# Optimization experiments

Measured on AMD Instinct MI355X. Metric: run time of the kernel, lower is better.

Reference implementation:

```python
import jax, jax.numpy as jnp
import numpy as np

N_NODES = 100000
N_EDGES = 3200000
NFEAT, NHID, NCLASS = 512, 256, 40


def spmm(edge_src, edge_dst, edge_w, h):
    # sparse adjacency @ h via gather + weighted segment-sum over destination nodes
    msgs = h[edge_src] * edge_w[:, None]          # [E, d]
    return jax.ops.segment_sum(msgs, edge_dst, num_segments=N_NODES)


def gcn_layer(h, W, b, edge_src, edge_dst, edge_w):
    support = h @ W                                # [N, d_out]
    return spmm(edge_src, edge_dst, edge_w, support) + b


def setup_inputs() -> dict:
    key = jax.random.key(0)
    ks = jax.random.split(key, 16)
    def w(k, shape, fan_in):
        return jax.random.normal(k, shape, dtype=jnp.float32) / np.sqrt(fan_in)
    inp = {
        'x': jax.random.normal(ks[0], (N_NODES, NFEAT), dtype=jnp.float32),
        'W1': w(ks[1], (NFEAT, NHID), NFEAT), 'b1': jnp.zeros((NHID,), jnp.float32),
        'W2': w(ks[2], (NHID, NHID), NHID),  'b2': jnp.zeros((NHID,), jnp.float32),
        'W3': w(ks[3], (NHID, NHID), NHID),  'b3': jnp.zeros((NHID,), jnp.float32),
        'W4': w(ks[4], (NHID, NHID), NHID),  'b4': jnp.zeros((NHID,), jnp.float32),
        'W5': w(ks[5], (NHID, NHID), NHID),  'b5': jnp.zeros((NHID,), jnp.float32),
        'W6': w(ks[6], (NHID, NCLASS), NHID),'b6': jnp.zeros((NCLASS,), jnp.float32),
        'edge_w': jax.random.uniform(ks[7], (N_EDGES,), dtype=jnp.float32),
        'edge_src': jax.random.randint(ks[8], (N_EDGES,), 0, N_NODES, dtype=jnp.int32),
        'edge_dst': jax.random.randint(ks[9], (N_EDGES,), 0, N_NODES, dtype=jnp.int32),
    }
    return inp


def reference(x, W1, b1, W2, b2, W3, b3, W4, b4, W5, b5, W6, b6,
              edge_w, edge_src, edge_dst):
    # eval mode: dropout is identity
    h = jax.nn.relu(gcn_layer(x, W1, b1, edge_src, edge_dst, edge_w))
    h = jax.nn.relu(gcn_layer(h, W2, b2, edge_src, edge_dst, edge_w))
    h = jax.nn.relu(gcn_layer(h, W3, b3, edge_src, edge_dst, edge_w))
    h = jax.nn.relu(gcn_layer(h, W4, b4, edge_src, edge_dst, edge_w))
    h = jax.nn.relu(gcn_layer(h, W5, b5, edge_src, edge_dst, edge_w))
    h = gcn_layer(h, W6, b6, edge_src, edge_dst, edge_w)
    return jax.nn.log_softmax(h, axis=1)
```

## Files before the change

### kernel.cpp

```cpp
#include <hip/hip_runtime.h>
#include <hip/hip_bf16.h>

static const int NN = 100000;
static const int NE = 3200000;
static const int F0 = 512;
static const int FH = 256;
static const int NC = 40;

#define CHUNK_SHIFT 13
static const int NCH  = (NN + (1 << CHUNK_SHIFT) - 1) >> CHUNK_SHIFT;
static const int KEYS = NN * NCH;

#define NPB_SHIFT 8
static const int NPB = 1 << NPB_SHIFT;
static const int NB  = (NN + NPB - 1) >> NPB_SHIFT;
static const int KPB = NPB * NCH;
#define EPB_A 8192

typedef __attribute__((ext_vector_type(8))) short bf16x8;
typedef __attribute__((ext_vector_type(16))) float f32x16;

__device__ __forceinline__ float bf2f(unsigned short u) {
    union { unsigned int i; float f; } c; c.i = ((unsigned int)u) << 16; return c.f;
}
__device__ __forceinline__ unsigned short f2bf(float f) {
    __hip_bfloat16 h = __float2bfloat16(f);
    return *reinterpret_cast<unsigned short*>(&h);
}

__global__ __launch_bounds__(256) void hist_bucket(const int* __restrict__ dst,
                                                   int* __restrict__ bcount, int E) {
    __shared__ int h[NB];
    for (int i = threadIdx.x; i < NB; i += 256) h[i] = 0;
    __syncthreads();
    for (int e = blockIdx.x * 256 + threadIdx.x; e < E; e += gridDim.x * 256)
        atomicAdd(&h[dst[e] >> NPB_SHIFT], 1);
    __syncthreads();
    for (int i = threadIdx.x; i < NB; i += 256)
        if (h[i]) atomicAdd(&bcount[i], h[i]);
}

__global__ __launch_bounds__(512) void scan_buckets(const int* __restrict__ bcount,
                                                    int* __restrict__ bstart,
                                                    int* __restrict__ bcursor, int E) {
    __shared__ int t[512];
    int tid = threadIdx.x;
    int v = (tid < NB) ? bcount[tid] : 0;
    t[tid] = v;
    __syncthreads();
    for (int off = 1; off < 512; off <<= 1) {
        int u = (tid >= off) ? t[tid - off] : 0;
        __syncthreads();
        t[tid] += u;
        __syncthreads();
    }
    if (tid < NB) {
        int s = t[tid] - v;
        bstart[tid] = s;
        bcursor[tid] = s;
    }
    if (tid == 0) bstart[NB] = E;
}

__global__ __launch_bounds__(256) void bin_scatter(const int* __restrict__ src,
                                                   const int* __restrict__ dst,
                                                   const float* __restrict__ w,
                                                   int* __restrict__ bcursor,
                                                   uint2* __restrict__ binned, int E) {
    __shared__ int hist[NB];
    __shared__ int base[NB];
    int tid = threadIdx.x;
    int e0 = blockIdx.x * EPB_A;
    int e1 = e0 + EPB_A; if (e1 > E) e1 = E;
    for (int i = tid; i < NB; i += 256) hist[i] = 0;
    __syncthreads();
    for (int e = e0 + tid; e < e1; e += 256)
        atomicAdd(&hist[dst[e] >> NPB_SHIFT], 1);
    __syncthreads();
    for (int i = tid; i < NB; i += 256) {
        int c = hist[i];
        base[i] = c ? atomicAdd(&bcursor[i], c) : 0;
        hist[i] = 0;
    }
    __syncthreads();
    for (int e = e0 + tid; e < e1; e += 256) {
        int d = dst[e];
        int b = d >> NPB_SHIFT;
        int off = atomicAdd(&hist[b], 1);
        unsigned int wq = (unsigned int)rintf(w[e] * 32767.f);
        unsigned int packed = ((unsigned int)src[e] << 15) | wq;
        binned[base[b] + off] = make_uint2(packed, (unsigned int)d);
    }
}

__global__ __launch_bounds__(256) void bin_sort(const uint2* __restrict__ binned,
                                                const int* __restrict__ bstart,
                                                int* __restrict__ keyStart,
                                                unsigned int* __restrict__ ev, int E) {
    __shared__ int hist[KPB];
    __shared__ int part[256];
    int b = blockIdx.x;
    int tid = threadIdx.x;
    int nodeLo = b << NPB_SHIFT;
    int eLo = bstart[b], eHi = bstart[b + 1];

    for (int i = tid; i < KPB; i += 256) hist[i] = 0;
    __syncthreads();
    for (int e = eLo + tid; e < eHi; e += 256) {
        uint2 r = binned[e];
        int lkey = ((int)r.y - nodeLo) * NCH + (int)(r.x >> (15 + CHUNK_SHIFT));
        atomicAdd(&hist[lkey], 1);
    }
    __syncthreads();

    int k0 = tid * NCH;
    int loc[NCH];
    int s = 0;
    #pragma unroll
    for (int j = 0; j < NCH; j++) { int c = hist[k0 + j]; loc[j] = s; s += c; }
    part[tid] = s;
    __syncthreads();
    for (int off = 1; off < 256; off <<= 1) {
        int u = (tid >= off) ? part[tid - off] : 0;
        __syncthreads();
        part[tid] += u;
        __syncthreads();
    }
    int excl = (tid > 0) ? part[tid - 1] : 0;
    __syncthreads();
    #pragma unroll
    for (int j = 0; j < NCH; j++) hist[k0 + j] = loc[j] + excl;
    __syncthreads();

    int keyBase = nodeLo * NCH;
    int kMax = KEYS - keyBase; if (kMax > KPB) kMax = KPB;
    for (int i = tid; i < kMax; i += 256) keyStart[keyBase + i] = eLo + hist[i];
    if (b == gridDim.x - 1 && tid == 0) keyStart[KEYS] = E;
    __syncthreads();

    for (int e = eLo + tid; e < eHi; e += 256) {
        uint2 r = binned[e];
        int lkey = ((int)r.y - nodeLo) * NCH + (int)(r.x >> (15 + CHUNK_SHIFT));
        int pos = eLo + atomicAdd(&hist[lkey], 1);
        ev[pos] = r.x;
    }
}

static const int TSEG0 = F0 * FH;
static const int TSEG1 = TSEG0 + FH * FH;
static const int TSEG2 = TSEG1 + FH * FH;
static const int TSEG3 = TSEG2 + FH * FH;
static const int TSEG4 = TSEG3 + FH * FH;
static const int TSEG5 = TSEG4 + FH * NC;

__global__ __launch_bounds__(256) void transpose_all(
        const float* __restrict__ W1, const float* __restrict__ W2,
        const float* __restrict__ W3, const float* __restrict__ W4,
        const float* __restrict__ W5, const float* __restrict__ W6,
        unsigned short* __restrict__ Wt1, unsigned short* __restrict__ Wt2,
        unsigned short* __restrict__ Wt3, unsigned short* __restrict__ Wt4,
        unsigned short* __restrict__ Wt5, unsigned short* __restrict__ Wt6) {
    int idx = blockIdx.x * 256 + threadIdx.x;
    if (idx >= TSEG5) return;
    const float* W; unsigned short* Wt; int K, N, i;
    if (idx < TSEG0)      { W = W1; Wt = Wt1; K = F0; N = FH; i = idx; }
    else if (idx < TSEG1) { W = W2; Wt = Wt2; K = FH; N = FH; i = idx - TSEG0; }
    else if (idx < TSEG2) { W = W3; Wt = Wt3; K = FH; N = FH; i = idx - TSEG1; }
    else if (idx < TSEG3) { W = W4; Wt = Wt4; K = FH; N = FH; i = idx - TSEG2; }
    else if (idx < TSEG4) { W = W5; Wt = Wt5; K = FH; N = FH; i = idx - TSEG3; }
    else                  { W = W6; Wt = Wt6; K = FH; N = NC; i = idx - TSEG4; }
    int n = i / K;
    int k = i - n * K;
    Wt[i] = f2bf(W[(size_t)k * N + n]);
}

template <int A_IS_F32>
__global__ __launch_bounds__(512, 2) void gemm_mfma_q(const void* __restrict__ Aptr,
                                                      const unsigned short* __restrict__ Wt,
                                                      unsigned char* __restrict__ Cq,
                                                      float* __restrict__ scales,
                                                      int M, int K) {
    __shared__ short Bs[65536];
    const int tid = threadIdx.x;
    const int w = tid >> 6;
    const int l = tid & 63;
    const int m0 = blockIdx.x * 256 + w * 32;
    const int lrow = l & 31;
    const int lgrp = l >> 5;
    int row_a = m0 + lrow;
    if (row_a > M - 1) row_a = M - 1;

    f32x16 acc[8] = {};

    for (int kt = 0; kt < K; kt += 256) {
        if (kt) __syncthreads();
        #pragma unroll
        for (int it = 0; it < 16; ++it) {
            int fid = it * 512 + tid;
            int c = fid & 255;
            int f = fid >> 8;
            bf16x8 v = *reinterpret_cast<const bf16x8*>(Wt + (size_t)c * K + kt + f * 8);
            *reinterpret_cast<bf16x8*>(&Bs[((f << 8) + c) * 8]) = v;
        }
        __syncthreads();

        for (int kk = 0; kk < 256; kk += 32) {
            bf16x8 a0, a1;
            if (A_IS_F32) {
                const float* p0 = (const float*)Aptr + (size_t)row_a * K + kt + kk + lgrp * 8;
                const float* p1 = p0 + 16;
                #pragma unroll
                for (int j = 0; j < 8; j++) a0[j] = (short)f2bf(p0[j]);
                #pragma unroll
                for (int j = 0; j < 8; j++) a1[j] = (short)f2bf(p1[j]);
            } else {
                const unsigned short* p = (const unsigned short*)Aptr + (size_t)row_a * K + kt + kk + lgrp * 8;
                a0 = *reinterpret_cast<const bf16x8*>(p);
                a1 = *reinterpret_cast<const bf16x8*>(p + 16);
            }
            const int fbase = kk >> 3;
            #pragma unroll
            for (int s = 0; s < 2; s++) {
                const short* bp = &Bs[((fbase + s * 2 + lgrp) << 8) * 8];
                bf16x8 a = s ? a1 : a0;
                #pragma unroll
                for (int nt = 0; nt < 8; nt++) {
                    bf16x8 b = *reinterpret_cast<const bf16x8*>(bp + (nt * 32 + lrow) * 8);
                    acc[nt] = __builtin_amdgcn_mfma_f32_32x32x16_bf16(a, b, acc[nt], 0, 0, 0);
                }
            }
        }
    }

    #pragma unroll
    for (int r = 0; r < 16; r++) {
        float vm = 0.f;
        #pragma unroll
        for (int nt = 0; nt < 8; nt++) vm = fmaxf(vm, fabsf(acc[nt][r]));
        #pragma unroll
        for (int off = 1; off < 32; off <<= 1) vm = fmaxf(vm, __shfl_xor(vm, off));
        int row = m0 + (r & 3) + 8 * (r >> 2) + 4 * lgrp;
        float inv = (vm > 0.f) ? 127.f / vm : 0.f;
        if (row < M) {
            if (lrow == 0) scales[row] = vm * (1.f / 127.f);
            #pragma unroll
            for (int nt = 0; nt < 8; nt++) {
                int q = (int)rintf(acc[nt][r] * inv) + 128;
                Cq[(size_t)row * 256 + nt * 32 + lrow] = (unsigned char)q;
            }
        }
    }
}

__global__ __launch_bounds__(256) void spmm_kernel(const unsigned char* __restrict__ supq,
                                                   const float* __restrict__ scales,
                                                   const unsigned int* __restrict__ ev,
                                                   const int* __restrict__ keyStart,
                                                   const float* __restrict__ bias,
                                                   unsigned short* __restrict__ out,
                                                   int M, int do_relu) {
    int node = blockIdx.x * 4 + (threadIdx.x >> 6);
    int l = threadIdx.x & 63;
    if (node >= M) return;
    const int g = l >> 4;
    const int lane16 = l & 15;
    const int boff = lane16 * 16;
    const int kb = node * NCH;
    int e0 = keyStart[kb], e1 = keyStart[kb + NCH];

    float acc[16] = {};
    float sw = 0.f;
    int e = e0 + g;
    for (; e + 4 < e1; e += 8) {
        unsigned int m0 = ev[e], m1 = ev[e + 4];
        int s0 = m0 >> 15, s1 = m1 >> 15;
        float w0 = (float)(m0 & 0x7fffu) * scales[s0];
        float w1 = (float)(m1 & 0x7fffu) * scales[s1];
        uint4 r0 = *(const uint4*)(supq + (size_t)s0 * 256 + boff);
        uint4 r1 = *(const uint4*)(supq + (size_t)s1 * 256 + boff);
        sw += w0 + w1;
        const unsigned int rr0[4] = {r0.x, r0.y, r0.z, r0.w};
        const unsigned int rr1[4] = {r1.x, r1.y, r1.z, r1.w};
        #pragma unroll
        for (int q = 0; q < 4; q++) {
            #pragma unroll
            for (int j = 0; j < 4; j++) {
                acc[q * 4 + j] += w0 * (float)((rr0[q] >> (8 * j)) & 0xffu)
                                + w1 * (float)((rr1[q] >> (8 * j)) & 0xffu);
            }
        }
    }
    for (; e < e1; e += 4) {
        unsigned int m0 = ev[e];
        int s0 = m0 >> 15;
        float w0 = (float)(m0 & 0x7fffu) * scales[s0];
        uint4 r0 = *(const uint4*)(supq + (size_t)s0 * 256 + boff);
        sw += w0;
        const unsigned int rr0[4] = {r0.x, r0.y, r0.z, r0.w};
        #pragma unroll
        for (int q = 0; q < 4; q++) {
            #pragma unroll
            for (int j = 0; j < 4; j++)
                acc[q * 4 + j] += w0 * (float)((rr0[q] >> (8 * j)) & 0xffu);
        }
    }

    #pragma unroll
    for (int j = 0; j < 16; j++) {
        acc[j] += __shfl_xor(acc[j], 16);
        acc[j] += __shfl_xor(acc[j], 32);
    }
    sw += __shfl_xor(sw, 16);
    sw += __shfl_xor(sw, 32);

    if (g == 0) {
        const float* bp = bias + boff;
        bf16x8 o0, o1;
        #pragma unroll
        for (int j = 0; j < 8; j++) {
            float v = (acc[j] - 128.f * sw) * (1.f / 32767.f) + bp[j];
            if (do_relu) v = fmaxf(v, 0.f);
            o0[j] = (short)f2bf(v);
        }
        #pragma unroll
        for (int j = 0; j < 8; j++) {
            float v = (acc[8 + j] - 128.f * sw) * (1.f / 32767.f) + bp[8 + j];
            if (do_relu) v = fmaxf(v, 0.f);
            o1[j] = (short)f2bf(v);
        }
        *reinterpret_cast<bf16x8*>(out + (size_t)node * 256 + boff) = o0;
        *reinterpret_cast<bf16x8*>(out + (size_t)node * 256 + boff + 8) = o1;
    }
}

__global__ __launch_bounds__(256) void gemm6_mfma(const unsigned short* __restrict__ h,
                                                  const unsigned short* __restrict__ Wt6,
                                                  unsigned short* __restrict__ sup6, int M) {
    __shared__ short Bs[64][40];
    const int tid = threadIdx.x;
    const int w = tid >> 6;
    const int l = tid & 63;
    const int m0 = blockIdx.x * 128 + w * 32;
    const int lrow = l & 31;
    const int lgrp = l >> 5;
    int row_a = m0 + lrow;
    if (row_a > M - 1) row_a = M - 1;

    f32x16 acc[2] = {};

    for (int kk = 0; kk < 256; kk += 32) {
        __syncthreads();
        {
            int r = tid >> 2, part = tid & 3;
            bf16x8 v = {};
            if (r < NC) v = *(const bf16x8*)(Wt6 + (size_t)r * 256 + kk + part * 8);
            *reinterpret_cast<bf16x8*>(&Bs[r][part * 8]) = v;
        }
        __syncthreads();

        #pragma unroll
        for (int s = 0; s < 2; s++) {
            const unsigned short* pa = h + (size_t)row_a * 256 + kk + s * 16 + lgrp * 8;
            bf16x8 a = *(const bf16x8*)pa;
            #pragma unroll
            for (int nt = 0; nt < 2; nt++) {
                bf16x8 b = *(const bf16x8*)(&Bs[nt * 32 + lrow][s * 16 + lgrp * 8]);
                acc[nt] = __builtin_amdgcn_mfma_f32_32x32x16_bf16(a, b, acc[nt], 0, 0, 0);
            }
        }
    }

    #pragma unroll
    for (int nt = 0; nt < 2; nt++) {
        #pragma unroll
        for (int r = 0; r < 16; r++) {
            int row = m0 + (r & 3) + 8 * (r >> 2) + 4 * lgrp;
            int col = nt * 32 + lrow;
            if (row < M && col < NC) sup6[(size_t)row * NC + col] = f2bf(acc[nt][r]);
        }
    }
}

__global__ __launch_bounds__(256) void spmm6_lsm(const unsigned short* __restrict__ sup6,
                                                 const unsigned int* __restrict__ ev,
                                                 const int* __restrict__ keyStart,
                                                 const float* __restrict__ b6,
                                                 float* __restrict__ out, int M) {
    int node = blockIdx.x * 4 + (threadIdx.x >> 6);
    int l = threadIdx.x & 63;
    if (node >= M) return;
    const int kb = node * NCH;
    int e0 = keyStart[kb], e1 = keyStart[kb + NCH];
    float acc = 0.f;
    bool active = (l < NC);
    int cix = active ? l : 0;
    int e = e0;
    for (; e + 4 <= e1; e += 4) {
        unsigned int m0 = ev[e], m1 = ev[e + 1], m2 = ev[e + 2], m3 = ev[e + 3];
        float v0 = bf2f(sup6[(size_t)(m0 >> 15) * NC + cix]);
        float v1 = bf2f(sup6[(size_t)(m1 >> 15) * NC + cix]);
        float v2 = bf2f(sup6[(size_t)(m2 >> 15) * NC + cix]);
        float v3 = bf2f(sup6[(size_t)(m3 >> 15) * NC + cix]);
        acc += (float)(m0 & 0x7fffu) * v0 + (float)(m1 & 0x7fffu) * v1
             + (float)(m2 & 0x7fffu) * v2 + (float)(m3 & 0x7fffu) * v3;
    }
    for (; e < e1; e++) {
        unsigned int m0 = ev[e];
        acc += (float)(m0 & 0x7fffu) * bf2f(sup6[(size_t)(m0 >> 15) * NC + cix]);
    }
    acc *= (1.f / 32767.f);

    float x = active ? (acc + b6[l]) : -__builtin_inff();
    float mx = x;
    #pragma unroll
    for (int off = 32; off > 0; off >>= 1) mx = fmaxf(mx, __shfl_xor(mx, off));
    float ex = active ? __expf(x - mx) : 0.f;
    float sm = ex;
    #pragma unroll
    for (int off = 32; off > 0; off >>= 1) sm += __shfl_xor(sm, off);
    if (active) out[(size_t)node * NC + l] = x - mx - __logf(sm);
}

extern "C" void kernel_launch(void* const* d_in, const int* in_sizes, int n_in,
                              void* d_out, int out_size, void* d_ws, size_t ws_size,
                              hipStream_t stream) {
    const float* x  = (const float*)d_in[0];
    const float* W1 = (const float*)d_in[1];  const float* b1 = (const float*)d_in[2];
    const float* W2 = (const float*)d_in[3];  const float* b2 = (const float*)d_in[4];
    const float* W3 = (const float*)d_in[5];  const float* b3 = (const float*)d_in[6];
    const float* W4 = (const float*)d_in[7];  const float* b4 = (const float*)d_in[8];
    const float* W5 = (const float*)d_in[9];  const float* b5 = (const float*)d_in[10];
    const float* W6 = (const float*)d_in[11]; const float* b6 = (const float*)d_in[12];
    const float* edge_w  = (const float*)d_in[13];
    const int* edge_src  = (const int*)d_in[14];
    const int* edge_dst  = (const int*)d_in[15];

    char* p = (char*)d_ws;
    auto alloc = [&](size_t bytes) -> char* {
        char* r = p;
        p += (bytes + 255) & ~(size_t)255;
        return r;
    };
    unsigned short* h_a = (unsigned short*)alloc((size_t)NN * FH * 2);
    unsigned short* h_b = (unsigned short*)alloc((size_t)NN * FH * 2);
    unsigned char* supq = (unsigned char*)alloc((size_t)NN * 256);
    float* scales       = (float*)alloc((size_t)NN * 4);
    unsigned int* ev    = (unsigned int*)alloc((size_t)NE * 4);
    int* keyStart  = (int*)alloc((size_t)(KEYS + 1) * 4);
    int* bcount    = (int*)alloc((size_t)NB * 4);
    int* bstart    = (int*)alloc((size_t)(NB + 1) * 4);
    int* bcursor   = (int*)alloc((size_t)NB * 4);
    unsigned short* Wt1 = (unsigned short*)alloc((size_t)FH * F0 * 2);
    unsigned short* Wt2 = (unsigned short*)alloc((size_t)FH * FH * 2);
    unsigned short* Wt3 = (unsigned short*)alloc((size_t)FH * FH * 2);
    unsigned short* Wt4 = (unsigned short*)alloc((size_t)FH * FH * 2);
    unsigned short* Wt5 = (unsigned short*)alloc((size_t)FH * FH * 2);
    unsigned short* Wt6 = (unsigned short*)alloc((size_t)NC * FH * 2);
    unsigned short* sup6 = h_b;
    uint2* binned = (uint2*)h_b;

    hipMemsetAsync(bcount, 0, (size_t)NB * 4, stream);
    hist_bucket<<<1024, 256, 0, stream>>>(edge_dst, bcount, NE);
    scan_buckets<<<1, 512, 0, stream>>>(bcount, bstart, bcursor, NE);
    bin_scatter<<<(NE + EPB_A - 1) / EPB_A, 256, 0, stream>>>(edge_src, edge_dst, edge_w,
                                                              bcursor, binned, NE);
    bin_sort<<<NB, 256, 0, stream>>>(binned, bstart, keyStart, ev, NE);

    transpose_all<<<(TSEG5 + 255) / 256, 256, 0, stream>>>(W1, W2, W3, W4, W5, W6,
                                                           Wt1, Wt2, Wt3, Wt4, Wt5, Wt6);

    const int gemmGrid = (NN + 255) / 256;
    const int g6Grid   = (NN + 127) / 128;
    const int rowGrid  = (NN + 3) / 4;

    gemm_mfma_q<1><<<gemmGrid, 512, 0, stream>>>(x, Wt1, supq, scales, NN, F0);
    spmm_kernel<<<rowGrid, 256, 0, stream>>>(supq, scales, ev, keyStart, b1, h_a, NN, 1);
    gemm_mfma_q<0><<<gemmGrid, 512, 0, stream>>>(h_a, Wt2, supq, scales, NN, FH);
    spmm_kernel<<<rowGrid, 256, 0, stream>>>(supq, scales, ev, keyStart, b2, h_b, NN, 1);
    gemm_mfma_q<0><<<gemmGrid, 512, 0, stream>>>(h_b, Wt3, supq, scales, NN, FH);
    spmm_kernel<<<rowGrid, 256, 0, stream>>>(supq, scales, ev, keyStart, b3, h_a, NN, 1);
    gemm_mfma_q<0><<<gemmGrid, 512, 0, stream>>>(h_a, Wt4, supq, scales, NN, FH);
    spmm_kernel<<<rowGrid, 256, 0, stream>>>(supq, scales, ev, keyStart, b4, h_b, NN, 1);
    gemm_mfma_q<0><<<gemmGrid, 512, 0, stream>>>(h_b, Wt5, supq, scales, NN, FH);
    spmm_kernel<<<rowGrid, 256, 0, stream>>>(supq, scales, ev, keyStart, b5, h_a, NN, 1);
    gemm6_mfma<<<g6Grid, 256, 0, stream>>>(h_a, Wt6, sup6, NN);
    spmm6_lsm<<<rowGrid, 256, 0, stream>>>(sup6, ev, keyStart, b6, (float*)d_out, NN);
}
```

Baseline: 1.144 ms.

## Split hidden-layer GEMM output columns across two blocks with per-half quantization scales

Hidden-layer GEMMs now launch twice as many blocks, each computing 128 of the 256 output columns with half the LDS and accumulator registers. This is meant to raise occupancy and parallelism on the MFMA GEMM. Each half gets its own int8 scale, so the scale array doubles in size and the SpMM picks a scale per lane half. The cost is that each A row is loaded twice, once per column half, and the SpMM does an extra indexed scale gather.

```diff
diff --git a/kernel.cpp b/kernel.cpp
--- a/kernel.cpp
+++ b/kernel.cpp
@@ -174,12 +174,11 @@
     Wt[i] = f2bf(W[(size_t)k * N + n]);
 }
 
-template <int A_IS_F32>
-__global__ __launch_bounds__(512, 2) void gemm_mfma_q(const void* __restrict__ Aptr,
-                                                      const unsigned short* __restrict__ Wt,
-                                                      unsigned char* __restrict__ Cq,
-                                                      float* __restrict__ scales,
-                                                      int M, int K) {
+__global__ __launch_bounds__(512, 2) void gemm_mfma_q_f32(const float* __restrict__ A,
+                                                          const unsigned short* __restrict__ Wt,
+                                                          unsigned char* __restrict__ Cq,
+                                                          float* __restrict__ scales,
+                                                          int M, int K) {
     __shared__ short Bs[65536];
     const int tid = threadIdx.x;
     const int w = tid >> 6;
@@ -206,18 +205,12 @@
 
         for (int kk = 0; kk < 256; kk += 32) {
             bf16x8 a0, a1;
-            if (A_IS_F32) {
-                const float* p0 = (const float*)Aptr + (size_t)row_a * K + kt + kk + lgrp * 8;
-                const float* p1 = p0 + 16;
-                #pragma unroll
-                for (int j = 0; j < 8; j++) a0[j] = (short)f2bf(p0[j]);
-                #pragma unroll
-                for (int j = 0; j < 8; j++) a1[j] = (short)f2bf(p1[j]);
-            } else {
-                const unsigned short* p = (const unsigned short*)Aptr + (size_t)row_a * K + kt + kk + lgrp * 8;
-                a0 = *reinterpret_cast<const bf16x8*>(p);
-                a1 = *reinterpret_cast<const bf16x8*>(p + 16);
-            }
+            const float* p0 = A + (size_t)row_a * K + kt + kk + lgrp * 8;
+            const float* p1 = p0 + 16;
+            #pragma unroll
+            for (int j = 0; j < 8; j++) a0[j] = (short)f2bf(p0[j]);
+            #pragma unroll
+            for (int j = 0; j < 8; j++) a1[j] = (short)f2bf(p1[j]);
             const int fbase = kk >> 3;
             #pragma unroll
             for (int s = 0; s < 2; s++) {
@@ -242,11 +235,81 @@
         int row = m0 + (r & 3) + 8 * (r >> 2) + 4 * lgrp;
         float inv = (vm > 0.f) ? 127.f / vm : 0.f;
         if (row < M) {
-            if (lrow == 0) scales[row] = vm * (1.f / 127.f);
+            if (lrow == 0) {
+                float sc = vm * (1.f / 127.f);
+                scales[row * 2]     = sc;
+                scales[row * 2 + 1] = sc;
+            }
             #pragma unroll
             for (int nt = 0; nt < 8; nt++) {
                 int q = (int)rintf(acc[nt][r] * inv) + 128;
                 Cq[(size_t)row * 256 + nt * 32 + lrow] = (unsigned char)q;
+            }
+        }
+    }
+}
+
+__global__ __launch_bounds__(512, 2) void gemm_mfma_q_cs(const unsigned short* __restrict__ A,
+                                                         const unsigned short* __restrict__ Wt,
+                                                         unsigned char* __restrict__ Cq,
+                                                         float* __restrict__ scales,
+                                                         int M) {
+    __shared__ short Bs[32768];
+    const int tid = threadIdx.x;
+    const int w = tid >> 6;
+    const int l = tid & 63;
+    const int tile = blockIdx.x >> 1;
+    const int ch = blockIdx.x & 1;
+    const int m0 = tile * 256 + w * 32;
+    const int lrow = l & 31;
+    const int lgrp = l >> 5;
+    int row_a = m0 + lrow;
+    if (row_a > M - 1) row_a = M - 1;
+
+    #pragma unroll
+    for (int it = 0; it < 8; ++it) {
+        int fid = it * 512 + tid;
+        int c = fid & 127;
+        int f = fid >> 7;
+        bf16x8 v = *reinterpret_cast<const bf16x8*>(Wt + (size_t)(ch * 128 + c) * 256 + f * 8);
+        *reinterpret_cast<bf16x8*>(&Bs[((f << 7) + c) * 8]) = v;
+    }
+    __syncthreads();
+
+    f32x16 acc[4] = {};
+
+    for (int kk = 0; kk < 256; kk += 32) {
+        const unsigned short* p = A + (size_t)row_a * 256 + kk + lgrp * 8;
+        bf16x8 a0 = *reinterpret_cast<const bf16x8*>(p);
+        bf16x8 a1 = *reinterpret_cast<const bf16x8*>(p + 16);
+        const int fbase = kk >> 3;
+        #pragma unroll
+        for (int s = 0; s < 2; s++) {
+            const short* bp = &Bs[((fbase + s * 2 + lgrp) << 7) * 8];
+            bf16x8 a = s ? a1 : a0;
+            #pragma unroll
+            for (int nt = 0; nt < 4; nt++) {
+                bf16x8 b = *reinterpret_cast<const bf16x8*>(bp + (nt * 32 + lrow) * 8);
+                acc[nt] = __builtin_amdgcn_mfma_f32_32x32x16_bf16(a, b, acc[nt], 0, 0, 0);
+            }
+        }
+    }
+
+    #pragma unroll
+    for (int r = 0; r < 16; r++) {
+        float vm = 0.f;
+        #pragma unroll
+        for (int nt = 0; nt < 4; nt++) vm = fmaxf(vm, fabsf(acc[nt][r]));
+        #pragma unroll
+        for (int off = 1; off < 32; off <<= 1) vm = fmaxf(vm, __shfl_xor(vm, off));
+        int row = m0 + (r & 3) + 8 * (r >> 2) + 4 * lgrp;
+        float inv = (vm > 0.f) ? 127.f / vm : 0.f;
+        if (row < M) {
+            if (lrow == 0) scales[row * 2 + ch] = vm * (1.f / 127.f);
+            #pragma unroll
+            for (int nt = 0; nt < 4; nt++) {
+                int q = (int)rintf(acc[nt][r] * inv) + 128;
+                Cq[(size_t)row * 256 + ch * 128 + nt * 32 + lrow] = (unsigned char)q;
             }
         }
     }
@@ -265,6 +328,7 @@
     const int g = l >> 4;
     const int lane16 = l & 15;
     const int boff = lane16 * 16;
+    const int shalf = lane16 >> 3;
     const int kb = node * NCH;
     int e0 = keyStart[kb], e1 = keyStart[kb + NCH];
 
@@ -274,8 +338,8 @@
     for (; e + 4 < e1; e += 8) {
         unsigned int m0 = ev[e], m1 = ev[e + 4];
         int s0 = m0 >> 15, s1 = m1 >> 15;
-        float w0 = (float)(m0 & 0x7fffu) * scales[s0];
-        float w1 = (float)(m1 & 0x7fffu) * scales[s1];
+        float w0 = (float)(m0 & 0x7fffu) * scales[(s0 << 1) + shalf];
+        float w1 = (float)(m1 & 0x7fffu) * scales[(s1 << 1) + shalf];
         uint4 r0 = *(const uint4*)(supq + (size_t)s0 * 256 + boff);
         uint4 r1 = *(const uint4*)(supq + (size_t)s1 * 256 + boff);
         sw += w0 + w1;
@@ -293,7 +357,7 @@
     for (; e < e1; e += 4) {
         unsigned int m0 = ev[e];
         int s0 = m0 >> 15;
-        float w0 = (float)(m0 & 0x7fffu) * scales[s0];
+        float w0 = (float)(m0 & 0x7fffu) * scales[(s0 << 1) + shalf];
         uint4 r0 = *(const uint4*)(supq + (size_t)s0 * 256 + boff);
         sw += w0;
         const unsigned int rr0[4] = {r0.x, r0.y, r0.z, r0.w};
@@ -444,7 +508,7 @@
     unsigned short* h_a = (unsigned short*)alloc((size_t)NN * FH * 2);
     unsigned short* h_b = (unsigned short*)alloc((size_t)NN * FH * 2);
     unsigned char* supq = (unsigned char*)alloc((size_t)NN * 256);
-    float* scales       = (float*)alloc((size_t)NN * 4);
+    float* scales       = (float*)alloc((size_t)NN * 2 * 4);
     unsigned int* ev    = (unsigned int*)alloc((size_t)NE * 4);
     int* keyStart  = (int*)alloc((size_t)(KEYS + 1) * 4);
     int* bcount    = (int*)alloc((size_t)NB * 4);
@@ -469,19 +533,20 @@
     transpose_all<<<(TSEG5 + 255) / 256, 256, 0, stream>>>(W1, W2, W3, W4, W5, W6,
                                                            Wt1, Wt2, Wt3, Wt4, Wt5, Wt6);
 
-    const int gemmGrid = (NN + 255) / 256;
+    const int g1Grid   = (NN + 255) / 256;
+    const int csGrid   = ((NN + 255) / 256) * 2;
     const int g6Grid   = (NN + 127) / 128;
     const int rowGrid  = (NN + 3) / 4;
 
-    gemm_mfma_q<1><<<gemmGrid, 512, 0, stream>>>(x, Wt1, supq, scales, NN, F0);
+    gemm_mfma_q_f32<<<g1Grid, 512, 0, stream>>>(x, Wt1, supq, scales, NN, F0);
     spmm_kernel<<<rowGrid, 256, 0, stream>>>(supq, scales, ev, keyStart, b1, h_a, NN, 1);
-    gemm_mfma_q<0><<<gemmGrid, 512, 0, stream>>>(h_a, Wt2, supq, scales, NN, FH);
+    gemm_mfma_q_cs<<<csGrid, 512, 0, stream>>>(h_a, Wt2, supq, scales, NN);
     spmm_kernel<<<rowGrid, 256, 0, stream>>>(supq, scales, ev, keyStart, b2, h_b, NN, 1);
-    gemm_mfma_q<0><<<gemmGrid, 512, 0, stream>>>(h_b, Wt3, supq, scales, NN, FH);
+    gemm_mfma_q_cs<<<csGrid, 512, 0, stream>>>(h_b, Wt3, supq, scales, NN);
     spmm_kernel<<<rowGrid, 256, 0, stream>>>(supq, scales, ev, keyStart, b3, h_a, NN, 1);
-    gemm_mfma_q<0><<<gemmGrid, 512, 0, stream>>>(h_a, Wt4, supq, scales, NN, FH);
+    gemm_mfma_q_cs<<<csGrid, 512, 0, stream>>>(h_a, Wt4, supq, scales, NN);
     spmm_kernel<<<rowGrid, 256, 0, stream>>>(supq, scales, ev, keyStart, b4, h_b, NN, 1);
-    gemm_mfma_q<0><<<gemmGrid, 512, 0, stream>>>(h_b, Wt5, supq, scales, NN, FH);
+    gemm_mfma_q_cs<<<csGrid, 512, 0, stream>>>(h_b, Wt5, supq, scales, NN);
     spmm_kernel<<<rowGrid, 256, 0, stream>>>(supq, scales, ev, keyStart, b5, h_a, NN, 1);
     gemm6_mfma<<<g6Grid, 256, 0, stream>>>(h_a, Wt6, sup6, NN);
     spmm6_lsm<<<rowGrid, 256, 0, stream>>>(sup6, ev, keyStart, b6, (float*)d_out, NN);
```

After: 1.160 ms. About the same (+1.4%).
